# Optimization experiments

Hardware: AMD Instinct MI355X
Metric: run time of the kernel (lower is better)

## Reference

```python
import jax, jax.numpy as jnp
import numpy as np
import math

B, S, D, H = 4, 2048, 512, 8
DK = D // H


def setup_inputs() -> dict:
    key = jax.random.key(0)
    ks = jax.random.split(key, 12)
    def lin(k, scale):
        return jax.random.normal(k, (D, D), dtype=jnp.float32) * scale
    s = 1.0 / math.sqrt(D)
    return {
        "q": jax.random.normal(ks[0], (B, S, D), dtype=jnp.float32),
        "k": jax.random.normal(ks[1], (B, S, D), dtype=jnp.float32),
        "v": jax.random.normal(ks[2], (B, S, D), dtype=jnp.float32),
        "mask": jax.random.randint(ks[3], (B, S, S), 0, 2, dtype=jnp.int32),
        "Wq": lin(ks[4], s), "bq": jnp.zeros((D,), jnp.float32),
        "Wk": lin(ks[5], s), "bk": jnp.zeros((D,), jnp.float32),
        "Wv": lin(ks[6], s), "bv": jnp.zeros((D,), jnp.float32),
        "Wo": lin(ks[7], s), "bo": jnp.zeros((D,), jnp.float32),
    }


def reference(q, k, v, mask, Wq, bq, Wk, bk, Wv, bv, Wo, bo):
    bs = q.shape[0]
    # torch Linear: y = x @ W.T + b
    qh = (q @ Wq.T + bq).reshape(bs, -1, H, DK).transpose(0, 2, 1, 3)  # [b,h,s,dk]
    kh = (k @ Wk.T + bk).reshape(bs, -1, H, DK).transpose(0, 2, 1, 3)
    vh = (v @ Wv.T + bv).reshape(bs, -1, H, DK).transpose(0, 2, 1, 3)
    scores = jnp.einsum("bhqd,bhkd->bhqk", qh, kh) / math.sqrt(DK)
    scores = jnp.where(mask[:, None, :, :] == 0, jnp.float32(-1e9), scores)
    scores = jax.nn.softmax(scores, axis=-1)
    # dropout p=0.0 -> identity
    concat = jnp.einsum("bhqk,bhkd->bhqd", scores, vh)
    concat = concat.transpose(0, 2, 1, 3).reshape(bs, -1, D)
    output = concat @ Wo.T + bo
    return (output, scores)
```

## Files before the change

kernel.cpp:

```cpp
#include <hip/hip_runtime.h>
#include <hip/hip_bf16.h>

#define B_ 4
#define S_ 2048
#define D_ 512
#define H_ 8
#define DK_ 64
#define M_ (B_*S_)

typedef float f32x4 __attribute__((ext_vector_type(4)));
typedef __bf16 bf16x8 __attribute__((ext_vector_type(8)));
typedef unsigned short u16x8 __attribute__((ext_vector_type(8)));

static __device__ __forceinline__ unsigned short f2bf(float x) {
    return __builtin_bit_cast(unsigned short, __float2bfloat16(x));
}
static __device__ __forceinline__ float bf2f(unsigned short u) {
    return __bfloat162float(__builtin_bit_cast(__hip_bfloat16, u));
}
static __device__ __forceinline__ bf16x8 ldfrag(const unsigned short* p) {
    return __builtin_bit_cast(bf16x8, *(const u16x8*)p);
}

__global__ __launch_bounds__(256) void proj_mfma_kernel(
    const float* __restrict__ X, const float* __restrict__ W,
    const float* __restrict__ bias, float* __restrict__ Yf32,
    unsigned short* __restrict__ Yhi, unsigned short* __restrict__ Ylo, int mode)
{
    __shared__ __align__(16) unsigned short sAh[128][40], sAl[128][40];
    __shared__ __align__(16) unsigned short sBh[128][40], sBl[128][40];

    const int tid  = threadIdx.x;
    const int m0   = blockIdx.x * 128;
    const int n0   = blockIdx.y * 128;
    const int lane = tid & 63, wv = tid >> 6;
    const int quad = lane >> 4, col = lane & 15;
    const int wr   = wv >> 1,  wc  = wv & 1;

    const int srow = tid >> 1;
    const int scol = (tid & 1) * 16;

    const float* pa = X + (size_t)(m0 + srow) * D_ + scol;
    const float* pb = W + (size_t)(n0 + srow) * D_ + scol;

    f32x4 acc[4][4] = {};

    auto split_write = [&](unsigned short (*Sh)[40], unsigned short (*Sl)[40],
                           const float4& x0, const float4& x1, int coff) {
        float f[8] = {x0.x, x0.y, x0.z, x0.w, x1.x, x1.y, x1.z, x1.w};
        u16x8 h, l;
        #pragma unroll
        for (int j = 0; j < 8; ++j) {
            const unsigned u = __builtin_bit_cast(unsigned, f[j]);
            h[j] = (unsigned short)(u >> 16);
            const float hf = __builtin_bit_cast(float, u & 0xFFFF0000u);
            l[j] = (unsigned short)(__builtin_bit_cast(unsigned, f[j] - hf) >> 16);
        }
        *(u16x8*)&Sh[srow][scol + coff] = h;
        *(u16x8*)&Sl[srow][scol + coff] = l;
    };

    float4 ra[4], rb[4];
    #pragma unroll
    for (int i = 0; i < 4; ++i) {
        ra[i] = *(const float4*)(pa + i * 4);
        rb[i] = *(const float4*)(pb + i * 4);
    }

    for (int kt = 0; kt < D_; kt += 32) {
        split_write(sAh, sAl, ra[0], ra[1], 0);
        split_write(sAh, sAl, ra[2], ra[3], 8);
        split_write(sBh, sBl, rb[0], rb[1], 0);
        split_write(sBh, sBl, rb[2], rb[3], 8);
        __syncthreads();

        if (kt + 32 < D_) {
            #pragma unroll
            for (int i = 0; i < 4; ++i) {
                ra[i] = *(const float4*)(pa + kt + 32 + i * 4);
                rb[i] = *(const float4*)(pb + kt + 32 + i * 4);
            }
        }

        bf16x8 ah[4], al[4], bh[4], bl[4];
        #pragma unroll
        for (int i = 0; i < 4; ++i) {
            ah[i] = ldfrag(&sAh[wr * 64 + i * 16 + col][quad * 8]);
            al[i] = ldfrag(&sAl[wr * 64 + i * 16 + col][quad * 8]);
            bh[i] = ldfrag(&sBh[wc * 64 + i * 16 + col][quad * 8]);
            bl[i] = ldfrag(&sBl[wc * 64 + i * 16 + col][quad * 8]);
        }
        #pragma unroll
        for (int mi = 0; mi < 4; ++mi)
            #pragma unroll
            for (int nj = 0; nj < 4; ++nj) {
                acc[mi][nj] = __builtin_amdgcn_mfma_f32_16x16x32_bf16(ah[mi], bh[nj], acc[mi][nj], 0, 0, 0);
                acc[mi][nj] = __builtin_amdgcn_mfma_f32_16x16x32_bf16(al[mi], bh[nj], acc[mi][nj], 0, 0, 0);
                acc[mi][nj] = __builtin_amdgcn_mfma_f32_16x16x32_bf16(ah[mi], bl[nj], acc[mi][nj], 0, 0, 0);
            }
        __syncthreads();
    }

    #pragma unroll
    for (int nj = 0; nj < 4; ++nj) {
        const int n  = n0 + wc * 64 + nj * 16 + col;
        const float bn = bias[n];
        #pragma unroll
        for (int mi = 0; mi < 4; ++mi) {
            #pragma unroll
            for (int r = 0; r < 4; ++r) {
                const int m  = m0 + wr * 64 + mi * 16 + quad * 4 + r;
                const float vv = acc[mi][nj][r] + bn;
                if (mode == 0) {
                    Yf32[(size_t)m * D_ + n] = vv;
                } else {
                    const int bi = m >> 11;
                    const int si = m & (S_ - 1);
                    const int h  = n >> 6;
                    const int dk = n & 63;
                    const size_t idx = (((size_t)bi * H_ + h) * S_ + si) * DK_ + dk;
                    const unsigned short hi = f2bf(vv);
                    Yhi[idx] = hi;
                    if (mode == 1) Ylo[idx] = f2bf(vv - bf2f(hi));
                }
            }
        }
    }
}

__global__ __launch_bounds__(256) void attn_mfma_kernel(
    const unsigned short* __restrict__ q_hi, const unsigned short* __restrict__ q_lo,
    const unsigned short* __restrict__ k_hi, const unsigned short* __restrict__ k_lo,
    const unsigned short* __restrict__ v_hi, const int* __restrict__ mask,
    float* __restrict__ scores, float* __restrict__ concat)
{
    __shared__ __align__(16) unsigned short sQh[64][72], sQl[64][72];
    __shared__ __align__(16) unsigned short sKh[64][72], sKl[64][72];
    __shared__ __align__(16) unsigned short sVt[64][72];
    __shared__ __align__(16) unsigned short sP[64][72];

    const int tid = threadIdx.x;
    const int q0 = blockIdx.x * 64;
    const int h = blockIdx.y, b = blockIdx.z;
    const size_t bh = (size_t)b * H_ + h;
    const int wv = tid >> 6, lane = tid & 63, quad = lane >> 4, col = lane & 15;

    const int sr = tid >> 2, sc = (tid & 3) * 16;

    {
        const u16x8* gh = (const u16x8*)(q_hi + (bh * S_ + q0 + sr) * DK_ + sc);
        const u16x8* gl = (const u16x8*)(q_lo + (bh * S_ + q0 + sr) * DK_ + sc);
        *(u16x8*)&sQh[sr][sc] = gh[0]; *(u16x8*)&sQh[sr][sc + 8] = gh[1];
        *(u16x8*)&sQl[sr][sc] = gl[0]; *(u16x8*)&sQl[sr][sc + 8] = gl[1];
    }

    const int* mbase = mask + (size_t)b * S_ * S_;

    auto compute_svals = [&](int kt, float sv[4][4]) {
        #pragma unroll
        for (int t = 0; t < 4; ++t) {
            f32x4 acc = {0.f, 0.f, 0.f, 0.f};
            #pragma unroll
            for (int kc = 0; kc < 64; kc += 32) {
                bf16x8 ah = ldfrag(&sQh[wv * 16 + col][kc + quad * 8]);
                bf16x8 al = ldfrag(&sQl[wv * 16 + col][kc + quad * 8]);
                bf16x8 bh = ldfrag(&sKh[t * 16 + col][kc + quad * 8]);
                bf16x8 bl = ldfrag(&sKl[t * 16 + col][kc + quad * 8]);
                acc = __builtin_amdgcn_mfma_f32_16x16x32_bf16(ah, bh, acc, 0, 0, 0);
                acc = __builtin_amdgcn_mfma_f32_16x16x32_bf16(ah, bl, acc, 0, 0, 0);
                acc = __builtin_amdgcn_mfma_f32_16x16x32_bf16(al, bh, acc, 0, 0, 0);
            }
            #pragma unroll
            for (int r = 0; r < 4; ++r) {
                const int qg = q0 + wv * 16 + quad * 4 + r;
                const int kg = kt * 64 + t * 16 + col;
                float s = acc[r] * 0.125f;
                if (mbase[(size_t)qg * S_ + kg] == 0) s = -1e9f;
                sv[t][r] = s;
            }
        }
    };

    float m_run[4], l_run[4];
    #pragma unroll
    for (int r = 0; r < 4; ++r) { m_run[r] = -1e30f; l_run[r] = 0.f; }

    for (int kt = 0; kt < 32; ++kt) {
        __syncthreads();
        {
            const u16x8* gh = (const u16x8*)(k_hi + (bh * S_ + kt * 64 + sr) * DK_ + sc);
            const u16x8* gl = (const u16x8*)(k_lo + (bh * S_ + kt * 64 + sr) * DK_ + sc);
            *(u16x8*)&sKh[sr][sc] = gh[0]; *(u16x8*)&sKh[sr][sc + 8] = gh[1];
            *(u16x8*)&sKl[sr][sc] = gl[0]; *(u16x8*)&sKl[sr][sc + 8] = gl[1];
        }
        __syncthreads();
        float sv[4][4];
        compute_svals(kt, sv);
        #pragma unroll
        for (int r = 0; r < 4; ++r) {
            float tm = fmaxf(fmaxf(sv[0][r], sv[1][r]), fmaxf(sv[2][r], sv[3][r]));
            #pragma unroll
            for (int mm = 1; mm < 16; mm <<= 1) tm = fmaxf(tm, __shfl_xor(tm, mm));
            const float nm = fmaxf(m_run[r], tm);
            float ts = __expf(sv[0][r] - nm) + __expf(sv[1][r] - nm)
                     + __expf(sv[2][r] - nm) + __expf(sv[3][r] - nm);
            #pragma unroll
            for (int mm = 1; mm < 16; mm <<= 1) ts += __shfl_xor(ts, mm);
            l_run[r] = l_run[r] * __expf(m_run[r] - nm) + ts;
            m_run[r] = nm;
        }
    }
    float inv_l[4];
    #pragma unroll
    for (int r = 0; r < 4; ++r) inv_l[r] = 1.f / l_run[r];

    f32x4 oacc[4] = {};
    for (int kt = 0; kt < 32; ++kt) {
        __syncthreads();
        {
            const u16x8* gh = (const u16x8*)(k_hi + (bh * S_ + kt * 64 + sr) * DK_ + sc);
            const u16x8* gl = (const u16x8*)(k_lo + (bh * S_ + kt * 64 + sr) * DK_ + sc);
            *(u16x8*)&sKh[sr][sc] = gh[0]; *(u16x8*)&sKh[sr][sc + 8] = gh[1];
            *(u16x8*)&sKl[sr][sc] = gl[0]; *(u16x8*)&sKl[sr][sc + 8] = gl[1];
            const u16x8* gv = (const u16x8*)(v_hi + (bh * S_ + kt * 64 + sr) * DK_ + sc);
            u16x8 a0 = gv[0], a1 = gv[1];
            #pragma unroll
            for (int i = 0; i < 8; ++i) { sVt[sc + i][sr] = a0[i]; sVt[sc + 8 + i][sr] = a1[i]; }
        }
        __syncthreads();
        float sv[4][4];
        compute_svals(kt, sv);
        #pragma unroll
        for (int t = 0; t < 4; ++t) {
            #pragma unroll
            for (int r = 0; r < 4; ++r) {
                const int qg = q0 + wv * 16 + quad * 4 + r;
                const int kg = kt * 64 + t * 16 + col;
                const float p = __expf(sv[t][r] - m_run[r]) * inv_l[r];
                scores[(bh * S_ + qg) * S_ + kg] = p;
                sP[wv * 16 + quad * 4 + r][t * 16 + col] = f2bf(p);
            }
        }
        #pragma unroll
        for (int to = 0; to < 4; ++to) {
            #pragma unroll
            for (int kc = 0; kc < 64; kc += 32) {
                bf16x8 a  = ldfrag(&sP[wv * 16 + col][kc + quad * 8]);
                bf16x8 bb = ldfrag(&sVt[to * 16 + col][kc + quad * 8]);
                oacc[to] = __builtin_amdgcn_mfma_f32_16x16x32_bf16(a, bb, oacc[to], 0, 0, 0);
            }
        }
    }

    #pragma unroll
    for (int to = 0; to < 4; ++to) {
        #pragma unroll
        for (int r = 0; r < 4; ++r) {
            const int qg = q0 + wv * 16 + quad * 4 + r;
            concat[((size_t)b * S_ + qg) * D_ + h * DK_ + to * 16 + col] = oacc[to][r];
        }
    }
}

extern "C" void kernel_launch(void* const* d_in, const int* in_sizes, int n_in,
                              void* d_out, int out_size, void* d_ws, size_t ws_size,
                              hipStream_t stream) {
    const float* q  = (const float*)d_in[0];
    const float* k  = (const float*)d_in[1];
    const float* v  = (const float*)d_in[2];
    const int* mask = (const int*)d_in[3];
    const float* Wq = (const float*)d_in[4];  const float* bq = (const float*)d_in[5];
    const float* Wk = (const float*)d_in[6];  const float* bk = (const float*)d_in[7];
    const float* Wv = (const float*)d_in[8];  const float* bv = (const float*)d_in[9];
    const float* Wo = (const float*)d_in[10]; const float* bo = (const float*)d_in[11];

    float* out    = (float*)d_out;
    float* scores = out + (size_t)B_ * S_ * D_;

    const size_t NH = (size_t)B_ * H_ * S_ * DK_;
    unsigned short* q_hi = (unsigned short*)d_ws;
    unsigned short* q_lo = q_hi + NH;
    unsigned short* k_hi = q_lo + NH;
    unsigned short* k_lo = k_hi + NH;
    unsigned short* v_hi = k_lo + NH;
    float* concat = (float*)(v_hi + NH);

    dim3 gg(M_ / 128, D_ / 128);
    proj_mfma_kernel<<<gg, 256, 0, stream>>>(q, Wq, bq, nullptr, q_hi, q_lo, 1);
    proj_mfma_kernel<<<gg, 256, 0, stream>>>(k, Wk, bk, nullptr, k_hi, k_lo, 1);
    proj_mfma_kernel<<<gg, 256, 0, stream>>>(v, Wv, bv, nullptr, v_hi, nullptr, 2);
    attn_mfma_kernel<<<dim3(S_ / 64, H_, B_), 256, 0, stream>>>(
        q_hi, q_lo, k_hi, k_lo, v_hi, mask, scores, concat);
    proj_mfma_kernel<<<gg, 256, 0, stream>>>(concat, Wo, bo, out, nullptr, nullptr, 0);
}
```

Before: 1.038 ms.

## Pre-split inputs to bf16 hi/lo, pack mask to bits, fuse QKV projection

Adds pre-pass kernels that split activations and weights into bf16 hi/lo arrays and pack the int32 mask into 64-bit ballot words. The three projections become one fused GEMM that loads tiles directly into LDS with global_load_lds. The attention kernel keeps Q fragments in registers, prefetches K/V tiles into registers one iteration ahead, reads mask bits instead of int32 values, and writes concat as hi/lo bf16 for the output GEMM. This removes the 2x pass of 64 MB int32 mask reads in attention and the in-loop conversion work, at the cost of extra kernels and workspace traffic.

```diff
diff --git a/kernel.cpp b/kernel.cpp
--- a/kernel.cpp
+++ b/kernel.cpp
@@ -22,106 +22,159 @@
     return __builtin_bit_cast(bf16x8, *(const u16x8*)p);
 }
 
-__global__ __launch_bounds__(256) void proj_mfma_kernel(
-    const float* __restrict__ X, const float* __restrict__ W,
-    const float* __restrict__ bias, float* __restrict__ Yf32,
-    unsigned short* __restrict__ Yhi, unsigned short* __restrict__ Ylo, int mode)
-{
-    __shared__ __align__(16) unsigned short sAh[128][40], sAl[128][40];
-    __shared__ __align__(16) unsigned short sBh[128][40], sBl[128][40];
-
-    const int tid  = threadIdx.x;
-    const int m0   = blockIdx.x * 128;
-    const int n0   = blockIdx.y * 128;
+typedef __attribute__((address_space(1))) const unsigned int gu32;
+typedef __attribute__((address_space(3))) unsigned int lu32;
+static __device__ __forceinline__ void gl_lds16(const unsigned short* g, unsigned short* l) {
+    __builtin_amdgcn_global_load_lds((gu32*)g, (lu32*)l, 16, 0, 0);
+}
+
+static __device__ __forceinline__ void split8(const float4 x0, const float4 x1,
+                                              u16x8& h, u16x8& l) {
+    float f[8] = {x0.x, x0.y, x0.z, x0.w, x1.x, x1.y, x1.z, x1.w};
+    #pragma unroll
+    for (int j = 0; j < 8; ++j) {
+        const unsigned u = __builtin_bit_cast(unsigned, f[j]);
+        h[j] = (unsigned short)(u >> 16);
+        const float hf = __builtin_bit_cast(float, u & 0xFFFF0000u);
+        l[j] = (unsigned short)(__builtin_bit_cast(unsigned, f[j] - hf) >> 16);
+    }
+}
+
+__global__ __launch_bounds__(256) void split_x3(
+    const float* __restrict__ xq, const float* __restrict__ xk, const float* __restrict__ xv,
+    unsigned short* __restrict__ qh, unsigned short* __restrict__ qlo,
+    unsigned short* __restrict__ kh, unsigned short* __restrict__ klo,
+    unsigned short* __restrict__ vh, unsigned short* __restrict__ vlo)
+{
+    const size_t t = (size_t)blockIdx.x * 256 + threadIdx.x;
+    const int z = blockIdx.y;
+    const float* in = z == 0 ? xq : z == 1 ? xk : xv;
+    unsigned short* oh = z == 0 ? qh : z == 1 ? kh : vh;
+    unsigned short* ol = z == 0 ? qlo : z == 1 ? klo : vlo;
+    const float4* p = (const float4*)(in + t * 8);
+    u16x8 hh, ll;
+    split8(p[0], p[1], hh, ll);
+    ((u16x8*)oh)[t] = hh;
+    ((u16x8*)ol)[t] = ll;
+}
+
+__global__ __launch_bounds__(256) void split_w4(
+    const float* __restrict__ Wq, const float* __restrict__ Wk,
+    const float* __restrict__ Wv, const float* __restrict__ Wo,
+    unsigned short* __restrict__ Wcat_h, unsigned short* __restrict__ Wcat_l,
+    unsigned short* __restrict__ Wo_h, unsigned short* __restrict__ Wo_l)
+{
+    const size_t t = (size_t)blockIdx.x * 256 + threadIdx.x;
+    const int z = blockIdx.y;
+    const float* in = z == 0 ? Wq : z == 1 ? Wk : z == 2 ? Wv : Wo;
+    unsigned short* oh = z < 3 ? Wcat_h + (size_t)z * 262144 : Wo_h;
+    unsigned short* ol = z < 3 ? Wcat_l + (size_t)z * 262144 : Wo_l;
+    const float4* p = (const float4*)(in + t * 8);
+    u16x8 hh, ll;
+    split8(p[0], p[1], hh, ll);
+    ((u16x8*)oh)[t] = hh;
+    ((u16x8*)ol)[t] = ll;
+}
+
+__global__ __launch_bounds__(256) void mask_pack(
+    const int* __restrict__ mask, unsigned long long* __restrict__ bits)
+{
+    const size_t t = (size_t)blockIdx.x * 256 + threadIdx.x;
+    const int m = mask[t];
+    const unsigned long long w = __ballot(m != 0);
+    if ((threadIdx.x & 63) == 0) bits[t >> 6] = w;
+}
+
+__global__ __launch_bounds__(256) void gemm_hl(
+    const unsigned short* __restrict__ qXh, const unsigned short* __restrict__ qXl,
+    const unsigned short* __restrict__ kXh, const unsigned short* __restrict__ kXl,
+    const unsigned short* __restrict__ vXh, const unsigned short* __restrict__ vXl,
+    const unsigned short* __restrict__ Wh, const unsigned short* __restrict__ Wl,
+    const float* __restrict__ b0, const float* __restrict__ b1, const float* __restrict__ b2,
+    float* __restrict__ Yf32,
+    unsigned short* __restrict__ q_hi, unsigned short* __restrict__ q_lo,
+    unsigned short* __restrict__ k_hi, unsigned short* __restrict__ k_lo,
+    unsigned short* __restrict__ v_hi, int fused)
+{
+    __shared__ unsigned short sAh[128 * 64], sAl[128 * 64];
+    __shared__ unsigned short sBh[64 * 64], sBl[64 * 64];
+
+    const int tid = threadIdx.x;
     const int lane = tid & 63, wv = tid >> 6;
     const int quad = lane >> 4, col = lane & 15;
-    const int wr   = wv >> 1,  wc  = wv & 1;
-
-    const int srow = tid >> 1;
-    const int scol = (tid & 1) * 16;
-
-    const float* pa = X + (size_t)(m0 + srow) * D_ + scol;
-    const float* pb = W + (size_t)(n0 + srow) * D_ + scol;
-
-    f32x4 acc[4][4] = {};
-
-    auto split_write = [&](unsigned short (*Sh)[40], unsigned short (*Sl)[40],
-                           const float4& x0, const float4& x1, int coff) {
-        float f[8] = {x0.x, x0.y, x0.z, x0.w, x1.x, x1.y, x1.z, x1.w};
-        u16x8 h, l;
-        #pragma unroll
-        for (int j = 0; j < 8; ++j) {
-            const unsigned u = __builtin_bit_cast(unsigned, f[j]);
-            h[j] = (unsigned short)(u >> 16);
-            const float hf = __builtin_bit_cast(float, u & 0xFFFF0000u);
-            l[j] = (unsigned short)(__builtin_bit_cast(unsigned, f[j] - hf) >> 16);
-        }
-        *(u16x8*)&Sh[srow][scol + coff] = h;
-        *(u16x8*)&Sl[srow][scol + coff] = l;
-    };
-
-    float4 ra[4], rb[4];
-    #pragma unroll
-    for (int i = 0; i < 4; ++i) {
-        ra[i] = *(const float4*)(pa + i * 4);
-        rb[i] = *(const float4*)(pb + i * 4);
-    }
-
-    for (int kt = 0; kt < D_; kt += 32) {
-        split_write(sAh, sAl, ra[0], ra[1], 0);
-        split_write(sAh, sAl, ra[2], ra[3], 8);
-        split_write(sBh, sBl, rb[0], rb[1], 0);
-        split_write(sBh, sBl, rb[2], rb[3], 8);
-        __syncthreads();
-
-        if (kt + 32 < D_) {
+    const int wm = wv >> 1, wn = wv & 1;
+    const int m0 = blockIdx.x * 128;
+    const int n0g = blockIdx.y * 64;
+    const int mat = fused ? (n0g >> 9) : 0;
+    const unsigned short* Xh = (!fused || mat == 0) ? qXh : (mat == 1 ? kXh : vXh);
+    const unsigned short* Xl = (!fused || mat == 0) ? qXl : (mat == 1 ? kXl : vXl);
+
+    const int lr = lane >> 3;
+    const int lc = (lane & 7) * 8;
+
+    f32x4 acc[4][2] = {};
+
+    for (int kt = 0; kt < D_; kt += 64) {
+        #pragma unroll
+        for (int i = 0; i < 4; ++i) {
+            const int row = wv * 32 + i * 8 + lr;
+            gl_lds16(Xh + (size_t)(m0 + row) * D_ + kt + lc, sAh + (size_t)(wv * 32 + i * 8) * 64);
+            gl_lds16(Xl + (size_t)(m0 + row) * D_ + kt + lc, sAl + (size_t)(wv * 32 + i * 8) * 64);
+        }
+        #pragma unroll
+        for (int i = 0; i < 2; ++i) {
+            const int row = wv * 16 + i * 8 + lr;
+            gl_lds16(Wh + (size_t)(n0g + row) * D_ + kt + lc, sBh + (size_t)(wv * 16 + i * 8) * 64);
+            gl_lds16(Wl + (size_t)(n0g + row) * D_ + kt + lc, sBl + (size_t)(wv * 16 + i * 8) * 64);
+        }
+        __syncthreads();
+
+        #pragma unroll
+        for (int kc = 0; kc < 64; kc += 32) {
+            bf16x8 ah[4], al[4], bh[2], bl[2];
             #pragma unroll
             for (int i = 0; i < 4; ++i) {
-                ra[i] = *(const float4*)(pa + kt + 32 + i * 4);
-                rb[i] = *(const float4*)(pb + kt + 32 + i * 4);
-            }
-        }
-
-        bf16x8 ah[4], al[4], bh[4], bl[4];
+                ah[i] = ldfrag(&sAh[(wm * 64 + i * 16 + col) * 64 + kc + quad * 8]);
+                al[i] = ldfrag(&sAl[(wm * 64 + i * 16 + col) * 64 + kc + quad * 8]);
+            }
+            #pragma unroll
+            for (int j = 0; j < 2; ++j) {
+                bh[j] = ldfrag(&sBh[(wn * 32 + j * 16 + col) * 64 + kc + quad * 8]);
+                bl[j] = ldfrag(&sBl[(wn * 32 + j * 16 + col) * 64 + kc + quad * 8]);
+            }
+            #pragma unroll
+            for (int i = 0; i < 4; ++i)
+                #pragma unroll
+                for (int j = 0; j < 2; ++j) {
+                    acc[i][j] = __builtin_amdgcn_mfma_f32_16x16x32_bf16(ah[i], bh[j], acc[i][j], 0, 0, 0);
+                    acc[i][j] = __builtin_amdgcn_mfma_f32_16x16x32_bf16(al[i], bh[j], acc[i][j], 0, 0, 0);
+                    acc[i][j] = __builtin_amdgcn_mfma_f32_16x16x32_bf16(ah[i], bl[j], acc[i][j], 0, 0, 0);
+                }
+        }
+        __syncthreads();
+    }
+
+    #pragma unroll
+    for (int j = 0; j < 2; ++j) {
+        const int ng = n0g + wn * 32 + j * 16 + col;
+        const int n = fused ? (ng & 511) : ng;
+        const float bias = fused ? (mat == 0 ? b0[n] : mat == 1 ? b1[n] : b2[n]) : b0[n];
         #pragma unroll
         for (int i = 0; i < 4; ++i) {
-            ah[i] = ldfrag(&sAh[wr * 64 + i * 16 + col][quad * 8]);
-            al[i] = ldfrag(&sAl[wr * 64 + i * 16 + col][quad * 8]);
-            bh[i] = ldfrag(&sBh[wc * 64 + i * 16 + col][quad * 8]);
-            bl[i] = ldfrag(&sBl[wc * 64 + i * 16 + col][quad * 8]);
-        }
-        #pragma unroll
-        for (int mi = 0; mi < 4; ++mi)
-            #pragma unroll
-            for (int nj = 0; nj < 4; ++nj) {
-                acc[mi][nj] = __builtin_amdgcn_mfma_f32_16x16x32_bf16(ah[mi], bh[nj], acc[mi][nj], 0, 0, 0);
-                acc[mi][nj] = __builtin_amdgcn_mfma_f32_16x16x32_bf16(al[mi], bh[nj], acc[mi][nj], 0, 0, 0);
-                acc[mi][nj] = __builtin_amdgcn_mfma_f32_16x16x32_bf16(ah[mi], bl[nj], acc[mi][nj], 0, 0, 0);
-            }
-        __syncthreads();
-    }
-
-    #pragma unroll
-    for (int nj = 0; nj < 4; ++nj) {
-        const int n  = n0 + wc * 64 + nj * 16 + col;
-        const float bn = bias[n];
-        #pragma unroll
-        for (int mi = 0; mi < 4; ++mi) {
             #pragma unroll
             for (int r = 0; r < 4; ++r) {
-                const int m  = m0 + wr * 64 + mi * 16 + quad * 4 + r;
-                const float vv = acc[mi][nj][r] + bn;
-                if (mode == 0) {
+                const int m = m0 + wm * 64 + i * 16 + quad * 4 + r;
+                const float vv = acc[i][j][r] + bias;
+                if (!fused) {
                     Yf32[(size_t)m * D_ + n] = vv;
                 } else {
-                    const int bi = m >> 11;
-                    const int si = m & (S_ - 1);
-                    const int h  = n >> 6;
-                    const int dk = n & 63;
-                    const size_t idx = (((size_t)bi * H_ + h) * S_ + si) * DK_ + dk;
+                    const int bi = m >> 11, si = m & (S_ - 1);
+                    const int hh = n >> 6, dk = n & 63;
+                    const size_t idx = (((size_t)bi * H_ + hh) * S_ + si) * DK_ + dk;
                     const unsigned short hi = f2bf(vv);
-                    Yhi[idx] = hi;
-                    if (mode == 1) Ylo[idx] = f2bf(vv - bf2f(hi));
+                    if (mat == 0)      { q_hi[idx] = hi; q_lo[idx] = f2bf(vv - bf2f(hi)); }
+                    else if (mat == 1) { k_hi[idx] = hi; k_lo[idx] = f2bf(vv - bf2f(hi)); }
+                    else               { v_hi[idx] = hi; }
                 }
             }
         }
@@ -131,10 +184,10 @@
 __global__ __launch_bounds__(256) void attn_mfma_kernel(
     const unsigned short* __restrict__ q_hi, const unsigned short* __restrict__ q_lo,
     const unsigned short* __restrict__ k_hi, const unsigned short* __restrict__ k_lo,
-    const unsigned short* __restrict__ v_hi, const int* __restrict__ mask,
-    float* __restrict__ scores, float* __restrict__ concat)
-{
-    __shared__ __align__(16) unsigned short sQh[64][72], sQl[64][72];
+    const unsigned short* __restrict__ v_hi, const unsigned long long* __restrict__ mbits,
+    float* __restrict__ scores,
+    unsigned short* __restrict__ ch, unsigned short* __restrict__ cl)
+{
     __shared__ __align__(16) unsigned short sKh[64][72], sKl[64][72];
     __shared__ __align__(16) unsigned short sVt[64][72];
     __shared__ __align__(16) unsigned short sP[64][72];
@@ -144,38 +197,46 @@
     const int h = blockIdx.y, b = blockIdx.z;
     const size_t bh = (size_t)b * H_ + h;
     const int wv = tid >> 6, lane = tid & 63, quad = lane >> 4, col = lane & 15;
-
     const int sr = tid >> 2, sc = (tid & 3) * 16;
 
+    bf16x8 qh[2], ql[2];
     {
-        const u16x8* gh = (const u16x8*)(q_hi + (bh * S_ + q0 + sr) * DK_ + sc);
-        const u16x8* gl = (const u16x8*)(q_lo + (bh * S_ + q0 + sr) * DK_ + sc);
-        *(u16x8*)&sQh[sr][sc] = gh[0]; *(u16x8*)&sQh[sr][sc + 8] = gh[1];
-        *(u16x8*)&sQl[sr][sc] = gl[0]; *(u16x8*)&sQl[sr][sc + 8] = gl[1];
-    }
-
-    const int* mbase = mask + (size_t)b * S_ * S_;
-
-    auto compute_svals = [&](int kt, float sv[4][4]) {
+        const size_t qb = (bh * S_ + q0 + wv * 16 + col) * DK_;
+        qh[0] = ldfrag(q_hi + qb + quad * 8);
+        qh[1] = ldfrag(q_hi + qb + 32 + quad * 8);
+        ql[0] = ldfrag(q_lo + qb + quad * 8);
+        ql[1] = ldfrag(q_lo + qb + 32 + quad * 8);
+    }
+
+    const size_t mrow_base = ((size_t)b * S_ + q0 + wv * 16 + quad * 4) * (S_ / 64);
+
+    u16x8 rkh[2], rkl[2], rv[2];
+    auto ld_k = [&](int kt) {
+        const u16x8* gh = (const u16x8*)(k_hi + (bh * S_ + kt * 64 + sr) * DK_ + sc);
+        const u16x8* gl = (const u16x8*)(k_lo + (bh * S_ + kt * 64 + sr) * DK_ + sc);
+        rkh[0] = gh[0]; rkh[1] = gh[1]; rkl[0] = gl[0]; rkl[1] = gl[1];
+    };
+    auto ld_v = [&](int kt) {
+        const u16x8* gv = (const u16x8*)(v_hi + (bh * S_ + kt * 64 + sr) * DK_ + sc);
+        rv[0] = gv[0]; rv[1] = gv[1];
+    };
+
+    auto compute_svals = [&](const unsigned long long* mw, float sv[4][4]) {
         #pragma unroll
         for (int t = 0; t < 4; ++t) {
             f32x4 acc = {0.f, 0.f, 0.f, 0.f};
             #pragma unroll
-            for (int kc = 0; kc < 64; kc += 32) {
-                bf16x8 ah = ldfrag(&sQh[wv * 16 + col][kc + quad * 8]);
-                bf16x8 al = ldfrag(&sQl[wv * 16 + col][kc + quad * 8]);
-                bf16x8 bh = ldfrag(&sKh[t * 16 + col][kc + quad * 8]);
-                bf16x8 bl = ldfrag(&sKl[t * 16 + col][kc + quad * 8]);
-                acc = __builtin_amdgcn_mfma_f32_16x16x32_bf16(ah, bh, acc, 0, 0, 0);
-                acc = __builtin_amdgcn_mfma_f32_16x16x32_bf16(ah, bl, acc, 0, 0, 0);
-                acc = __builtin_amdgcn_mfma_f32_16x16x32_bf16(al, bh, acc, 0, 0, 0);
+            for (int kci = 0; kci < 2; ++kci) {
+                bf16x8 bhf = ldfrag(&sKh[t * 16 + col][kci * 32 + quad * 8]);
+                bf16x8 blf = ldfrag(&sKl[t * 16 + col][kci * 32 + quad * 8]);
+                acc = __builtin_amdgcn_mfma_f32_16x16x32_bf16(qh[kci], bhf, acc, 0, 0, 0);
+                acc = __builtin_amdgcn_mfma_f32_16x16x32_bf16(qh[kci], blf, acc, 0, 0, 0);
+                acc = __builtin_amdgcn_mfma_f32_16x16x32_bf16(ql[kci], bhf, acc, 0, 0, 0);
             }
             #pragma unroll
             for (int r = 0; r < 4; ++r) {
-                const int qg = q0 + wv * 16 + quad * 4 + r;
-                const int kg = kt * 64 + t * 16 + col;
                 float s = acc[r] * 0.125f;
-                if (mbase[(size_t)qg * S_ + kg] == 0) s = -1e9f;
+                if (!((mw[r] >> (t * 16 + col)) & 1ull)) s = -1e9f;
                 sv[t][r] = s;
             }
         }
@@ -185,17 +246,18 @@
     #pragma unroll
     for (int r = 0; r < 4; ++r) { m_run[r] = -1e30f; l_run[r] = 0.f; }
 
+    ld_k(0);
     for (int kt = 0; kt < 32; ++kt) {
         __syncthreads();
-        {
-            const u16x8* gh = (const u16x8*)(k_hi + (bh * S_ + kt * 64 + sr) * DK_ + sc);
-            const u16x8* gl = (const u16x8*)(k_lo + (bh * S_ + kt * 64 + sr) * DK_ + sc);
-            *(u16x8*)&sKh[sr][sc] = gh[0]; *(u16x8*)&sKh[sr][sc + 8] = gh[1];
-            *(u16x8*)&sKl[sr][sc] = gl[0]; *(u16x8*)&sKl[sr][sc + 8] = gl[1];
-        }
-        __syncthreads();
+        *(u16x8*)&sKh[sr][sc] = rkh[0]; *(u16x8*)&sKh[sr][sc + 8] = rkh[1];
+        *(u16x8*)&sKl[sr][sc] = rkl[0]; *(u16x8*)&sKl[sr][sc + 8] = rkl[1];
+        __syncthreads();
+        if (kt < 31) ld_k(kt + 1);
+        unsigned long long mw[4];
+        #pragma unroll
+        for (int r = 0; r < 4; ++r) mw[r] = mbits[mrow_base + (size_t)r * (S_ / 64) + kt];
         float sv[4][4];
-        compute_svals(kt, sv);
+        compute_svals(mw, sv);
         #pragma unroll
         for (int r = 0; r < 4; ++r) {
             float tm = fmaxf(fmaxf(sv[0][r], sv[1][r]), fmaxf(sv[2][r], sv[3][r]));
@@ -215,21 +277,20 @@
     for (int r = 0; r < 4; ++r) inv_l[r] = 1.f / l_run[r];
 
     f32x4 oacc[4] = {};
+    ld_k(0); ld_v(0);
     for (int kt = 0; kt < 32; ++kt) {
         __syncthreads();
-        {
-            const u16x8* gh = (const u16x8*)(k_hi + (bh * S_ + kt * 64 + sr) * DK_ + sc);
-            const u16x8* gl = (const u16x8*)(k_lo + (bh * S_ + kt * 64 + sr) * DK_ + sc);
-            *(u16x8*)&sKh[sr][sc] = gh[0]; *(u16x8*)&sKh[sr][sc + 8] = gh[1];
-            *(u16x8*)&sKl[sr][sc] = gl[0]; *(u16x8*)&sKl[sr][sc + 8] = gl[1];
-            const u16x8* gv = (const u16x8*)(v_hi + (bh * S_ + kt * 64 + sr) * DK_ + sc);
-            u16x8 a0 = gv[0], a1 = gv[1];
-            #pragma unroll
-            for (int i = 0; i < 8; ++i) { sVt[sc + i][sr] = a0[i]; sVt[sc + 8 + i][sr] = a1[i]; }
-        }
-        __syncthreads();
+        *(u16x8*)&sKh[sr][sc] = rkh[0]; *(u16x8*)&sKh[sr][sc + 8] = rkh[1];
+        *(u16x8*)&sKl[sr][sc] = rkl[0]; *(u16x8*)&sKl[sr][sc + 8] = rkl[1];
+        #pragma unroll
+        for (int i = 0; i < 8; ++i) { sVt[sc + i][sr] = rv[0][i]; sVt[sc + 8 + i][sr] = rv[1][i]; }
+        __syncthreads();
+        if (kt < 31) { ld_k(kt + 1); ld_v(kt + 1); }
+        unsigned long long mw[4];
+        #pragma unroll
+        for (int r = 0; r < 4; ++r) mw[r] = mbits[mrow_base + (size_t)r * (S_ / 64) + kt];
         float sv[4][4];
-        compute_svals(kt, sv);
+        compute_svals(mw, sv);
         #pragma unroll
         for (int t = 0; t < 4; ++t) {
             #pragma unroll
@@ -257,7 +318,11 @@
         #pragma unroll
         for (int r = 0; r < 4; ++r) {
             const int qg = q0 + wv * 16 + quad * 4 + r;
-            concat[((size_t)b * S_ + qg) * D_ + h * DK_ + to * 16 + col] = oacc[to][r];
+            const size_t idx = ((size_t)b * S_ + qg) * D_ + h * DK_ + to * 16 + col;
+            const float o = oacc[to][r];
+            const unsigned short oh16 = f2bf(o);
+            ch[idx] = oh16;
+            cl[idx] = f2bf(o - bf2f(oh16));
         }
     }
 }
@@ -278,18 +343,34 @@
     float* scores = out + (size_t)B_ * S_ * D_;
 
     const size_t NH = (size_t)B_ * H_ * S_ * DK_;
-    unsigned short* q_hi = (unsigned short*)d_ws;
-    unsigned short* q_lo = q_hi + NH;
-    unsigned short* k_hi = q_lo + NH;
-    unsigned short* k_lo = k_hi + NH;
-    unsigned short* v_hi = k_lo + NH;
-    float* concat = (float*)(v_hi + NH);
-
-    dim3 gg(M_ / 128, D_ / 128);
-    proj_mfma_kernel<<<gg, 256, 0, stream>>>(q, Wq, bq, nullptr, q_hi, q_lo, 1);
-    proj_mfma_kernel<<<gg, 256, 0, stream>>>(k, Wk, bk, nullptr, k_hi, k_lo, 1);
-    proj_mfma_kernel<<<gg, 256, 0, stream>>>(v, Wv, bv, nullptr, v_hi, nullptr, 2);
+    unsigned short* W = (unsigned short*)d_ws;
+    unsigned short* q_hi = W + 0 * NH;
+    unsigned short* q_lo = W + 1 * NH;
+    unsigned short* k_hi = W + 2 * NH;
+    unsigned short* k_lo = W + 3 * NH;
+    unsigned short* v_hi = W + 4 * NH;
+    unsigned short* qXh = W + 7 * NH;  unsigned short* qXl = W + 8 * NH;
+    unsigned short* kXh = W + 9 * NH;  unsigned short* kXl = W + 10 * NH;
+    unsigned short* vXh = W + 11 * NH; unsigned short* vXl = W + 12 * NH;
+    unsigned short* cat_h = qXh;       unsigned short* cat_l = qXl;
+    unsigned short* Wcat_h = W + 13 * NH;
+    unsigned short* Wcat_l = Wcat_h + 786432;
+    unsigned short* Wo_h   = Wcat_l + 786432;
+    unsigned short* Wo_l   = Wo_h + 262144;
+    unsigned long long* mbits = (unsigned long long*)(Wo_l + 262144);
+
+    split_x3<<<dim3(2048, 3), 256, 0, stream>>>(q, k, v, qXh, qXl, kXh, kXl, vXh, vXl);
+    split_w4<<<dim3(128, 4), 256, 0, stream>>>(Wq, Wk, Wv, Wo, Wcat_h, Wcat_l, Wo_h, Wo_l);
+    mask_pack<<<dim3(65536), 256, 0, stream>>>(mask, mbits);
+
+    gemm_hl<<<dim3(64, 24), 256, 0, stream>>>(
+        qXh, qXl, kXh, kXl, vXh, vXl, Wcat_h, Wcat_l, bq, bk, bv,
+        nullptr, q_hi, q_lo, k_hi, k_lo, v_hi, 1);
+
     attn_mfma_kernel<<<dim3(S_ / 64, H_, B_), 256, 0, stream>>>(
-        q_hi, q_lo, k_hi, k_lo, v_hi, mask, scores, concat);
-    proj_mfma_kernel<<<gg, 256, 0, stream>>>(concat, Wo, bo, out, nullptr, nullptr, 0);
-}
+        q_hi, q_lo, k_hi, k_lo, v_hi, mbits, scores, cat_h, cat_l);
+
+    gemm_hl<<<dim3(64, 8), 256, 0, stream>>>(
+        cat_h, cat_l, nullptr, nullptr, nullptr, nullptr, Wo_h, Wo_l, bo, nullptr, nullptr,
+        out, nullptr, nullptr, nullptr, nullptr, nullptr, 0);
+}
```

After: 1.030 ms. Within noise of the previous version (-0.8%).
